# Kernel tuning notes

Hardware: AMD Instinct MI355X
Metric: run time of the kernel (lower is better)

The kernel has to match this reference:

```python
import jax, jax.numpy as jnp
import numpy as np

N_GRAPHS = 32
N_NODES = 2048          # nodes per graph == lstm1 input_size
N_TOTAL = N_GRAPHS * N_NODES
N_EDGES = 1048576
HEADS = 8
GAT_OUT = 12            # per-head GAT output dim (== num_features)
OUT_CH = 9
NEG_SLOPE = 0.2
BN_EPS = 1e-5


def setup_inputs() -> dict:
    key = jax.random.key(0)
    ks = jax.random.split(key, 20)
    inp = {}
    inp['x'] = jax.random.normal(ks[0], (N_TOTAL, GAT_OUT), jnp.float32)
    inp['edge_index'] = jax.random.randint(ks[1], (2, N_EDGES), 0, N_TOTAL, jnp.int64)
    inp['W_gat'] = jax.random.normal(ks[2], (GAT_OUT, HEADS * GAT_OUT), jnp.float32) * 0.3
    inp['a_src'] = jax.random.normal(ks[3], (HEADS, GAT_OUT), jnp.float32) * 0.3
    inp['a_dst'] = jax.random.normal(ks[4], (HEADS, GAT_OUT), jnp.float32) * 0.3
    inp['gat_bias'] = jax.random.normal(ks[5], (GAT_OUT,), jnp.float32) * 0.1
    inp['bn_gamma'] = jax.random.uniform(ks[6], (GAT_OUT,), jnp.float32, 0.5, 1.5)
    inp['bn_beta'] = jax.random.normal(ks[7], (GAT_OUT,), jnp.float32) * 0.1
    inp['bn_mean'] = jax.random.normal(ks[8], (GAT_OUT,), jnp.float32) * 0.1
    inp['bn_var'] = jax.random.uniform(ks[9], (GAT_OUT,), jnp.float32, 0.5, 1.5)
    inp['w_ih1'] = jax.random.normal(ks[10], (4 * 32, N_NODES), jnp.float32) / np.sqrt(N_NODES)
    inp['w_hh1'] = jax.random.normal(ks[11], (4 * 32, 32), jnp.float32) / np.sqrt(32)
    inp['b_ih1'] = jnp.zeros((4 * 32,), jnp.float32)
    inp['b_hh1'] = jnp.zeros((4 * 32,), jnp.float32)
    inp['w_ih2'] = jax.random.normal(ks[12], (4 * 128, 32), jnp.float32) / np.sqrt(32)
    inp['w_hh2'] = jax.random.normal(ks[13], (4 * 128, 128), jnp.float32) / np.sqrt(128)
    inp['b_ih2'] = jnp.zeros((4 * 128,), jnp.float32)
    inp['b_hh2'] = jnp.zeros((4 * 128,), jnp.float32)
    inp['lin_w'] = jax.random.normal(ks[14], (N_NODES, 128), jnp.float32) / np.sqrt(128)
    inp['lin_b'] = jax.random.normal(ks[15], (N_NODES,), jnp.float32) * 0.1
    return inp


def _gat(x, edge_index, W, a_src, a_dst, bias):
    # PyG GATConv, heads=HEADS, out=GAT_OUT, concat=False (mean over heads), eval mode.
    N = x.shape[0]
    xp = (x @ W).reshape(N, HEADS, GAT_OUT)               # [N,H,C]
    loops = jnp.arange(N, dtype=edge_index.dtype)
    src = jnp.concatenate([edge_index[0], loops])
    dst = jnp.concatenate([edge_index[1], loops])
    asrc = jnp.einsum('nhc,hc->nh', xp, a_src)            # [N,H]
    adst = jnp.einsum('nhc,hc->nh', xp, a_dst)
    e = jax.nn.leaky_relu(asrc[src] + adst[dst], NEG_SLOPE)  # [E,H]
    m = jax.ops.segment_max(e, dst, num_segments=N)
    e = jnp.exp(e - m[dst])
    denom = jax.ops.segment_sum(e, dst, num_segments=N)
    alpha = e / (denom[dst] + 1e-16)
    msg = xp[src] * alpha[:, :, None]                     # [E,H,C]
    out = jax.ops.segment_sum(msg, dst, num_segments=N)   # [N,H,C]
    return out.mean(axis=1) + bias                        # concat=False -> head mean


def _lstm(x_seq, w_ih, w_hh, b_ih, b_hh):
    # x_seq: [T,B,I]; PyTorch gate order i,f,g,o.
    Hh = w_hh.shape[1]
    B = x_seq.shape[1]
    bias = b_ih + b_hh

    def step(carry, xt):
        h, c = carry
        gates = xt @ w_ih.T + h @ w_hh.T + bias
        i, f, g, o = jnp.split(gates, 4, axis=-1)
        c = jax.nn.sigmoid(f) * c + jax.nn.sigmoid(i) * jnp.tanh(g)
        h = jax.nn.sigmoid(o) * jnp.tanh(c)
        return (h, c), h

    init = (jnp.zeros((B, Hh), x_seq.dtype), jnp.zeros((B, Hh), x_seq.dtype))
    _, hs = jax.lax.scan(step, init, x_seq)
    return hs


def reference(x, edge_index, W_gat, a_src, a_dst, gat_bias,
              bn_gamma, bn_beta, bn_mean, bn_var,
              w_ih1, w_hh1, b_ih1, b_hh1,
              w_ih2, w_hh2, b_ih2, b_hh2,
              lin_w, lin_b):
    h = _gat(x, edge_index, W_gat, a_src, a_dst, gat_bias)          # [N,12]
    h = (h - bn_mean) / jnp.sqrt(bn_var + BN_EPS) * bn_gamma + bn_beta
    # dropout inactive in eval mode
    h = jax.nn.log_softmax(h, axis=1)
    h = h.reshape(N_GRAPHS, N_NODES, GAT_OUT)
    h = jnp.moveaxis(h, 2, 0)                                       # [T=12,B,n]
    h = _lstm(h, w_ih1, w_hh1, b_ih1, b_hh1)                        # [12,B,32]
    h = _lstm(h, w_ih2, w_hh2, b_ih2, b_hh2)                        # [12,B,128]
    h = h @ lin_w.T + lin_b                                         # [12,B,n]
    h = h[-OUT_CH:]                                                 # [9,B,n]
    h = jnp.moveaxis(h, 0, 2)                                       # [B,n,9]
    return h.reshape(N_GRAPHS * N_NODES, OUT_CH)
```

## Files before the change

kernel.cpp:

```cpp
#include <hip/hip_runtime.h>
#include <math.h>

#define N_EDGES_C 1048576
#define N_TOTAL_C 65536

typedef _Float16 h2v __attribute__((ext_vector_type(2)));
typedef int i4v __attribute__((ext_vector_type(4)));

#if defined(__has_builtin)
#if __has_builtin(__builtin_amdgcn_fdot2)
#define HAS_FDOT2 1
#endif
#endif

__device__ __forceinline__ float fdot2(h2v a, h2v b, float c) {
#ifdef HAS_FDOT2
    return __builtin_amdgcn_fdot2(a, b, c, false);
#else
    return c + (float)a.x * (float)b.x + (float)a.y * (float)b.y;
#endif
}

__device__ __forceinline__ float sigf(float x){ return 1.0f/(1.0f+expf(-x)); }
__device__ __forceinline__ float lrelu(float x){ return (x>=0.f)? x : 0.2f*x; }


__global__ void prep_kernel(const float* __restrict__ x, const float* __restrict__ Wg,
                            const float* __restrict__ a_src, const float* __restrict__ a_dst,
                            _Float16* __restrict__ xpp)
{
    int tid = threadIdx.x;
    __shared__ float Ws[12*96];
    __shared__ float as_s[96], ad_s[96];
    for (int i = tid; i < 1152; i += 256) Ws[i] = Wg[i];
    if (tid < 96) { as_s[tid] = a_src[tid]; ad_s[tid] = a_dst[tid]; }
    __syncthreads();
    int gid = blockIdx.x * 256 + tid;
    int n = gid >> 3;
    int h = gid & 7;
    const float4* xv = (const float4*)(x + (size_t)n * 12);
    float4 v0 = xv[0], v1 = xv[1], v2 = xv[2];
    float xr[12] = {v0.x,v0.y,v0.z,v0.w, v1.x,v1.y,v1.z,v1.w, v2.x,v2.y,v2.z,v2.w};
    float xp_[12];
    #pragma unroll
    for (int c = 0; c < 12; c++) {
        float acc = 0.f;
        #pragma unroll
        for (int k = 0; k < 12; k++) acc += xr[k] * Ws[k*96 + h*12 + c];
        xp_[c] = acc;
    }
    float sa = 0.f, sd = 0.f;
    #pragma unroll
    for (int c = 0; c < 12; c++) { sa += xp_[c]*as_s[h*12+c]; sd += xp_[c]*ad_s[h*12+c]; }
    union { _Float16 hh[16]; float ff[8]; float4 f4[2]; } s;
    #pragma unroll
    for (int c = 0; c < 12; c++) s.hh[c] = (_Float16)xp_[c];
    s.ff[6] = sa;
    s.ff[7] = sd;
    float4* o = (float4*)(xpp + (size_t)gid * 16);
    o[0] = s.f4[0];
    o[1] = s.f4[1];
}

__global__ __launch_bounds__(256)
void edge_hist(const int* __restrict__ ei, unsigned* __restrict__ cnt,
               unsigned* __restrict__ rank8)
{
    __shared__ unsigned hist[16384];
    int tid = threadIdx.x;
    int slice = blockIdx.x;
    for (int i = tid; i < 16384; i += 256) hist[i] = 0;
    __syncthreads();
    const i4v* dst4 = (const i4v*)(ei + N_EDGES_C) + slice*2048;
    for (int i = tid; i < 2048; i += 256) {
        i4v d = __builtin_nontemporal_load(&dst4[i]);
        int dd[4] = {d.x, d.y, d.z, d.w};
        unsigned packed = 0;
        #pragma unroll
        for (int j = 0; j < 4; j++) {
            int dj = dd[j];
            unsigned sh = (unsigned)(dj & 3) << 3;
            unsigned old = atomicAdd(&hist[dj >> 2], 1u << sh);
            packed |= ((old >> sh) & 0xffu) << (j*8);
        }
        __builtin_nontemporal_store(packed, &rank8[slice*2048 + i]);
    }
    __syncthreads();
    unsigned* cg = cnt + (size_t)slice*16384;
    for (int i = tid; i < 16384; i += 256) cg[i] = hist[i];
}

__global__ void slice_prefix(unsigned* __restrict__ cnt, int* __restrict__ deg)
{
    int w = blockIdx.x*256 + threadIdx.x;
    unsigned run = 0;
    unsigned* base = cnt + w;
    for (int s = 0; s < 128; s++) {
        unsigned v = base[(size_t)s*16384];
        base[(size_t)s*16384] = run;
        run += v;
    }
    ((int4*)deg)[w] = make_int4((int)(run & 255u), (int)((run >> 8) & 255u),
                                (int)((run >> 16) & 255u), (int)(run >> 24));
}

__global__ void scan_build(const int* __restrict__ deg, int* __restrict__ rowptr)
{
    __shared__ int sums[1024];
    int tid = threadIdx.x;
    int4 v[16];
    const int4* deg4 = (const int4*)deg;
    #pragma unroll
    for (int j = 0; j < 16; j++) v[j] = deg4[tid*16 + j];
    int s = 0;
    #pragma unroll
    for (int j = 0; j < 16; j++) s += v[j].x + v[j].y + v[j].z + v[j].w;
    sums[tid] = s;
    __syncthreads();
    for (int off = 1; off < 1024; off <<= 1) {
        int t = 0;
        if (tid >= off) t = sums[tid - off];
        __syncthreads();
        if (tid >= off) sums[tid] += t;
        __syncthreads();
    }
    int run = sums[tid] - s;
    int4* rp4 = (int4*)rowptr;
    #pragma unroll
    for (int j = 0; j < 16; j++) {
        int4 r;
        r.x = run; run += v[j].x;
        r.y = run; run += v[j].y;
        r.z = run; run += v[j].z;
        r.w = run; run += v[j].w;
        rp4[tid*16 + j] = r;
    }
    if (tid == 1023) rowptr[65536] = run;
}

__global__ void edge_scatter(const int* __restrict__ ei, const unsigned* __restrict__ rank8,
                             const unsigned* __restrict__ cnt, const int* __restrict__ rowptr,
                             int* __restrict__ csr)
{
    int g8 = blockIdx.x & 7;
    int slice = (blockIdx.x >> 3) & 127;
    int half = blockIdx.x >> 10;
    int base = slice*2048 + half*1024;
    const i4v* dst4 = (const i4v*)(ei + N_EDGES_C);
    const i4v* src4 = (const i4v*)ei;
    const unsigned* cslice = cnt + (size_t)slice*16384;
    for (int i = threadIdx.x; i < 1024; i += 256) {
        int idx = base + i;
        i4v d = __builtin_nontemporal_load(&dst4[idx]);
        i4v s = __builtin_nontemporal_load(&src4[idx]);
        unsigned r = __builtin_nontemporal_load(&rank8[idx]);
        int dd[4] = {d.x, d.y, d.z, d.w};
        int ss[4] = {s.x, s.y, s.z, s.w};
        #pragma unroll
        for (int j = 0; j < 4; j++) {
            int dj = dd[j];
            if ((dj >> 13) == g8) {
                unsigned word = cslice[dj >> 2];
                int so = (int)((word >> ((unsigned)(dj & 3) << 3)) & 0xffu);
                int rk = (int)((r >> (j*8)) & 0xffu);
                csr[rowptr[dj] + so + rk] = ss[j];
            }
        }
    }
}

__global__ void gat_aggregate(const _Float16* __restrict__ xpp,
                              const int* __restrict__ rowptr, const int* __restrict__ csr_src,
                              const float* __restrict__ gat_bias, const float* __restrict__ bn_gamma,
                              const float* __restrict__ bn_beta, const float* __restrict__ bn_mean,
                              const float* __restrict__ bn_var, float* __restrict__ seq)
{
    int gid = blockIdx.x * 256 + threadIdx.x;
    int n = gid >> 3;
    int h = gid & 7;

    float acc[12];
    float adst_n, d;
    {
        const float4* p = (const float4*)(xpp + (size_t)n*128 + h*16);
        float4 f0 = p[0], f1 = p[1];
        adst_n = f1.w;
        float w = __expf(lrelu(f1.z + adst_n));
        d = w;
        h2v c0 = __builtin_bit_cast(h2v, f0.x), c1 = __builtin_bit_cast(h2v, f0.y);
        h2v c2 = __builtin_bit_cast(h2v, f0.z), c3 = __builtin_bit_cast(h2v, f0.w);
        h2v c4 = __builtin_bit_cast(h2v, f1.x), c5 = __builtin_bit_cast(h2v, f1.y);
        acc[0]=w*(float)c0.x; acc[1]=w*(float)c0.y; acc[2]=w*(float)c1.x; acc[3]=w*(float)c1.y;
        acc[4]=w*(float)c2.x; acc[5]=w*(float)c2.y; acc[6]=w*(float)c3.x; acc[7]=w*(float)c3.y;
        acc[8]=w*(float)c4.x; acc[9]=w*(float)c4.y; acc[10]=w*(float)c5.x; acc[11]=w*(float)c5.y;
    }

    auto accum = [&](float4 f0, float4 f1) {
        float w = __expf(lrelu(f1.z + adst_n));
        d += w;
        h2v c0 = __builtin_bit_cast(h2v, f0.x), c1 = __builtin_bit_cast(h2v, f0.y);
        h2v c2 = __builtin_bit_cast(h2v, f0.z), c3 = __builtin_bit_cast(h2v, f0.w);
        h2v c4 = __builtin_bit_cast(h2v, f1.x), c5 = __builtin_bit_cast(h2v, f1.y);
        acc[0]+=w*(float)c0.x; acc[1]+=w*(float)c0.y; acc[2]+=w*(float)c1.x; acc[3]+=w*(float)c1.y;
        acc[4]+=w*(float)c2.x; acc[5]+=w*(float)c2.y; acc[6]+=w*(float)c3.x; acc[7]+=w*(float)c3.y;
        acc[8]+=w*(float)c4.x; acc[9]+=w*(float)c4.y; acc[10]+=w*(float)c5.x; acc[11]+=w*(float)c5.y;
    };

    int beg = rowptr[n], end = rowptr[n+1];
    const _Float16* xh = xpp + (size_t)h * 16;
    int i = beg;
    for (; i + 4 <= end; i += 4) {
        int s0 = csr_src[i+0];
        int s1 = csr_src[i+1];
        int s2 = csr_src[i+2];
        int s3 = csr_src[i+3];
        const float4* p0 = (const float4*)(xh + (size_t)s0*128);
        const float4* p1 = (const float4*)(xh + (size_t)s1*128);
        const float4* p2 = (const float4*)(xh + (size_t)s2*128);
        const float4* p3 = (const float4*)(xh + (size_t)s3*128);
        float4 a0 = p0[0], b0 = p0[1];
        float4 a1 = p1[0], b1 = p1[1];
        float4 a2 = p2[0], b2 = p2[1];
        float4 a3 = p3[0], b3 = p3[1];
        accum(a0, b0);
        accum(a1, b1);
        accum(a2, b2);
        accum(a3, b3);
    }
    for (; i < end; i++) {
        int src = csr_src[i];
        const float4* p = (const float4*)(xh + (size_t)src*128);
        float4 f0 = p[0], f1 = p[1];
        accum(f0, f1);
    }

    float inv = 1.0f / (d + 1e-16f);
    float res[12];
    #pragma unroll
    for (int c = 0; c < 12; c++) {
        float v = acc[c] * inv;
        v += __shfl_xor(v, 1);
        v += __shfl_xor(v, 2);
        v += __shfl_xor(v, 4);
        res[c] = v * 0.125f;
    }
    if (h == 0) {
        float vals[12];
        float mx = -1e30f;
        #pragma unroll
        for (int c = 0; c < 12; c++) {
            float v = res[c] + gat_bias[c];
            v = (v - bn_mean[c]) * rsqrtf(bn_var[c] + 1e-5f) * bn_gamma[c] + bn_beta[c];
            vals[c] = v;
            mx = fmaxf(mx, v);
        }
        float sum = 0.f;
        #pragma unroll
        for (int c = 0; c < 12; c++) sum += __expf(vals[c] - mx);
        float lse = __logf(sum) + mx;
        #pragma unroll
        for (int c = 0; c < 12; c++) seq[(size_t)c * N_TOTAL_C + n] = vals[c] - lse;
    }
}

__global__ void gemm_x1(const float* __restrict__ A, const float* __restrict__ B,
                        float* __restrict__ C)
{
    __shared__ float As[32][33], Bs[32][33];
    const int K = 2048, N = 128;
    int tid = threadIdx.x;
    int tx = tid & 31, ty = tid >> 5;
    int bm = blockIdx.x * 32, bn = blockIdx.y * 32;
    int kbase = blockIdx.z * 128;
    float acc[4] = {0.f,0.f,0.f,0.f};
    for (int kk = 0; kk < 128; kk += 32) {
        int k0 = kbase + kk;
        #pragma unroll
        for (int i = 0; i < 4; i++) {
            int r = ty + i*8;
            As[r][tx] = A[(size_t)(bm + r) * K + k0 + tx];
            Bs[r][tx] = B[(size_t)(bn + r) * K + k0 + tx];
        }
        __syncthreads();
        #pragma unroll
        for (int k = 0; k < 32; k++) {
            float bv = Bs[tx][k];
            #pragma unroll
            for (int i = 0; i < 4; i++) acc[i] += As[ty + i*8][k] * bv;
        }
        __syncthreads();
    }
    #pragma unroll
    for (int i = 0; i < 4; i++)
        atomicAdd(&C[(size_t)(bm + ty + i*8) * N + bn + tx], acc[i]);
}

__global__ __launch_bounds__(512)
void lstm_fused(const float* __restrict__ X1, const float* __restrict__ w_hh1,
                const float* __restrict__ b_ih1, const float* __restrict__ b_hh1,
                const float* __restrict__ w_ih2, const float* __restrict__ w_hh2,
                const float* __restrict__ b_ih2, const float* __restrict__ b_hh2,
                float* __restrict__ H2)
{
    __shared__ float whh1[128*33];
    __shared__ float b1s[128];
    __shared__ float h1[32], c1[32];
    __shared__ __align__(16) _Float16 h1s[32];
    __shared__ __align__(16) _Float16 h2s[128];
    __shared__ float c2[128];
    __shared__ float g1s[128], g2s[512];
    int tid = threadIdx.x;
    int b = blockIdx.x;

    h2v whh[64];
    {
        const float2* wh = (const float2*)(w_hh2 + (size_t)tid * 128);
        #pragma unroll
        for (int k = 0; k < 64; k++) {
            float2 v = wh[k];
            h2v t; t.x = (_Float16)v.x; t.y = (_Float16)v.y;
            whh[k] = t;
        }
    }
    h2v wih[16];
    {
        const float2* wi = (const float2*)(w_ih2 + (size_t)tid * 32);
        #pragma unroll
        for (int k = 0; k < 16; k++) {
            float2 v = wi[k];
            h2v t; t.x = (_Float16)v.x; t.y = (_Float16)v.y;
            wih[k] = t;
        }
    }
    float b2 = b_ih2[tid] + b_hh2[tid];

    for (int i = tid; i < 128*32; i += 512) whh1[(i >> 5)*33 + (i & 31)] = w_hh1[i];
    if (tid < 128) b1s[tid] = b_ih1[tid] + b_hh1[tid];
    if (tid < 32)  { h1[tid] = 0.f; c1[tid] = 0.f; h1s[tid] = (_Float16)0.f; }
    if (tid < 128) { c2[tid] = 0.f; h2s[tid] = (_Float16)0.f; }
    __syncthreads();

    for (int t = 0; t < 12; t++) {
        float p0 = b2, p1 = 0.f, p2 = 0.f, p3 = 0.f;
        #pragma unroll
        for (int j = 0; j < 16; j++) {
            float4 f = ((const float4*)h2s)[j];
            p0 = fdot2(__builtin_bit_cast(h2v, f.x), whh[j*4+0], p0);
            p1 = fdot2(__builtin_bit_cast(h2v, f.y), whh[j*4+1], p1);
            p2 = fdot2(__builtin_bit_cast(h2v, f.z), whh[j*4+2], p2);
            p3 = fdot2(__builtin_bit_cast(h2v, f.w), whh[j*4+3], p3);
        }
        float acc2 = (p0 + p1) + (p2 + p3);

        if (tid < 128) {
            const float* wr = &whh1[tid * 33];
            float acc = X1[((size_t)t*32 + b)*128 + tid] + b1s[tid];
            #pragma unroll
            for (int k = 0; k < 32; k++) acc += h1[k] * wr[k];
            g1s[tid] = acc;
        }
        __syncthreads();
        if (tid < 32) {
            float ig = sigf(g1s[tid]), fg = sigf(g1s[32+tid]);
            float gg = tanhf(g1s[64+tid]), og = sigf(g1s[96+tid]);
            float cn = fg * c1[tid] + ig * gg;
            c1[tid] = cn;
            float hn = og * tanhf(cn);
            h1[tid] = hn;
            h1s[tid] = (_Float16)hn;
        }
        __syncthreads();
        {
            float q0 = 0.f, q1 = 0.f, q2 = 0.f, q3 = 0.f;
            #pragma unroll
            for (int j = 0; j < 4; j++) {
                float4 f = ((const float4*)h1s)[j];
                q0 = fdot2(__builtin_bit_cast(h2v, f.x), wih[j*4+0], q0);
                q1 = fdot2(__builtin_bit_cast(h2v, f.y), wih[j*4+1], q1);
                q2 = fdot2(__builtin_bit_cast(h2v, f.z), wih[j*4+2], q2);
                q3 = fdot2(__builtin_bit_cast(h2v, f.w), wih[j*4+3], q3);
            }
            g2s[tid] = acc2 + (q0 + q1) + (q2 + q3);
        }
        __syncthreads();
        if (tid < 128) {
            float ig = sigf(g2s[tid]), fg = sigf(g2s[128+tid]);
            float gg = tanhf(g2s[256+tid]), og = sigf(g2s[384+tid]);
            float cn = fg * c2[tid] + ig * gg;
            c2[tid] = cn;
            float hn = og * tanhf(cn);
            h2s[tid] = (_Float16)hn;
            if (t >= 3) H2[((size_t)t*32 + b)*128 + tid] = hn;
        }
        __syncthreads();
    }
}

__global__ void gemm_out(const float* __restrict__ A, const float* __restrict__ B,
                         const float* __restrict__ bias, float* __restrict__ out)
{
    __shared__ float As[32][33], Bs[32][33];
    const int K = 128;
    int tid = threadIdx.x;
    int tx = tid & 31, ty = tid >> 5;
    int bm = blockIdx.x * 32, bn = blockIdx.y * 32;
    float acc[4] = {0.f,0.f,0.f,0.f};
    for (int k0 = 0; k0 < K; k0 += 32) {
        #pragma unroll
        for (int i = 0; i < 4; i++) {
            int r = ty + i*8;
            As[r][tx] = A[(size_t)(bm + r) * K + k0 + tx];
            Bs[r][tx] = B[(size_t)(bn + r) * K + k0 + tx];
        }
        __syncthreads();
        #pragma unroll
        for (int kk = 0; kk < 32; kk++) {
            float bv = Bs[tx][kk];
            #pragma unroll
            for (int i = 0; i < 4; i++) acc[i] += As[ty + i*8][kk] * bv;
        }
        __syncthreads();
    }
    int j = blockIdx.x;
    int nn = bn + tx;
    float bv = bias[nn];
    #pragma unroll
    for (int i = 0; i < 4; i++) {
        int bb = ty + i*8;
        out[((size_t)bb * 2048 + nn) * 9 + j] = acc[i] + bv;
    }
}

extern "C" void kernel_launch(void* const* d_in, const int* in_sizes, int n_in,
                              void* d_out, int out_size, void* d_ws, size_t ws_size,
                              hipStream_t stream)
{
    const float* x        = (const float*)d_in[0];
    const int*   ei       = (const int*)  d_in[1];
    const float* W_gat    = (const float*)d_in[2];
    const float* a_src    = (const float*)d_in[3];
    const float* a_dst    = (const float*)d_in[4];
    const float* gat_bias = (const float*)d_in[5];
    const float* bn_gamma = (const float*)d_in[6];
    const float* bn_beta  = (const float*)d_in[7];
    const float* bn_mean  = (const float*)d_in[8];
    const float* bn_var   = (const float*)d_in[9];
    const float* w_ih1    = (const float*)d_in[10];
    const float* w_hh1    = (const float*)d_in[11];
    const float* b_ih1    = (const float*)d_in[12];
    const float* b_hh1    = (const float*)d_in[13];
    const float* w_ih2    = (const float*)d_in[14];
    const float* w_hh2    = (const float*)d_in[15];
    const float* b_ih2    = (const float*)d_in[16];
    const float* b_hh2    = (const float*)d_in[17];
    const float* lin_w    = (const float*)d_in[18];
    const float* lin_b    = (const float*)d_in[19];
    float* out = (float*)d_out;

    float* ws = (float*)d_ws;
    _Float16* xpp = (_Float16*)ws;
    float* seq  = ws + 4194304;
    float* X1   = seq + 786432;
    float* H2   = X1  + 49152;
    int* rowptr = (int*)(H2 + 49152);
    int* deg    = rowptr + 65544;
    unsigned* cnt = (unsigned*)(deg + 65536);
    unsigned* rank8 = cnt + 2097152;
    int* csr    = (int*)(rank8 + 262144);

    hipMemsetAsync(X1, 0, 49152 * sizeof(float), stream);
    prep_kernel <<<2048, 256, 0, stream>>>(x, W_gat, a_src, a_dst, xpp);
    edge_hist   <<<128, 256, 0, stream>>>(ei, cnt, rank8);
    slice_prefix<<<64, 256, 0, stream>>>(cnt, deg);
    scan_build  <<<1, 1024, 0, stream>>>(deg, rowptr);
    edge_scatter<<<2048, 256, 0, stream>>>(ei, rank8, cnt, rowptr, csr);
    gat_aggregate<<<2048, 256, 0, stream>>>(xpp, rowptr, csr,
                                            gat_bias, bn_gamma, bn_beta, bn_mean, bn_var, seq);
    gemm_x1<<<dim3(12, 4, 16), 256, 0, stream>>>(seq, w_ih1, X1);
    lstm_fused<<<32, 512, 0, stream>>>(X1, w_hh1, b_ih1, b_hh1, w_ih2, w_hh2, b_ih2, b_hh2, H2);
    gemm_out<<<dim3(9, 64), 256, 0, stream>>>(H2 + 96*128, lin_w, lin_b, out);
}
```

Measured before the change: 272.5 us.

## Stage edge scatter in LDS, prefetch LSTM inputs, use fast sigmoid/tanh

edge_scatter no longer has each of 8 group blocks re-read the same edges. Each block now reads its quarter-slice once, computes destination positions into shared memory tagged with a group id, then writes csr in 8 group-ordered passes. This cuts redundant global edge reads at the cost of LDS staging and a barrier. The LSTM kernel prefetches the next step's X1 value into a register and replaces expf/tanhf with __expf plus a hardware reciprocal, which lowers accuracy slightly. slice_prefix is relaunched with 128x128 threads instead of 64x256.

```diff
diff --git a/kernel.cpp b/kernel.cpp
--- a/kernel.cpp
+++ b/kernel.cpp
@@ -10,6 +10,9 @@
 #if defined(__has_builtin)
 #if __has_builtin(__builtin_amdgcn_fdot2)
 #define HAS_FDOT2 1
+#endif
+#if __has_builtin(__builtin_amdgcn_rcpf)
+#define HAS_RCPF 1
 #endif
 #endif
 
@@ -21,7 +24,15 @@
 #endif
 }
 
-__device__ __forceinline__ float sigf(float x){ return 1.0f/(1.0f+expf(-x)); }
+__device__ __forceinline__ float fast_rcp(float x) {
+#ifdef HAS_RCPF
+    return __builtin_amdgcn_rcpf(x);
+#else
+    return 1.0f / x;
+#endif
+}
+__device__ __forceinline__ float sigf(float x){ return fast_rcp(1.0f + __expf(-x)); }
+__device__ __forceinline__ float tanh_fast(float x){ return fmaf(2.0f, fast_rcp(1.0f + __expf(-2.0f*x)), -1.0f); }
 __device__ __forceinline__ float lrelu(float x){ return (x>=0.f)? x : 0.2f*x; }
 
 
@@ -92,7 +103,7 @@
 
 __global__ void slice_prefix(unsigned* __restrict__ cnt, int* __restrict__ deg)
 {
-    int w = blockIdx.x*256 + threadIdx.x;
+    int w = blockIdx.x*128 + threadIdx.x;
     unsigned run = 0;
     unsigned* base = cnt + w;
     for (int s = 0; s < 128; s++) {
@@ -138,18 +149,20 @@
     if (tid == 1023) rowptr[65536] = run;
 }
 
-__global__ void edge_scatter(const int* __restrict__ ei, const unsigned* __restrict__ rank8,
-                             const unsigned* __restrict__ cnt, const int* __restrict__ rowptr,
-                             int* __restrict__ csr)
-{
-    int g8 = blockIdx.x & 7;
-    int slice = (blockIdx.x >> 3) & 127;
-    int half = blockIdx.x >> 10;
-    int base = slice*2048 + half*1024;
+__global__ __launch_bounds__(256)
+void edge_scatter(const int* __restrict__ ei, const unsigned* __restrict__ rank8,
+                  const unsigned* __restrict__ cnt, const int* __restrict__ rowptr,
+                  int* __restrict__ csr)
+{
+    __shared__ unsigned pos_s[2048];
+    __shared__ int src_s[2048];
+    int slice = blockIdx.x >> 2;
+    int quar  = blockIdx.x & 3;
+    int base = slice*2048 + quar*512;
     const i4v* dst4 = (const i4v*)(ei + N_EDGES_C);
     const i4v* src4 = (const i4v*)ei;
     const unsigned* cslice = cnt + (size_t)slice*16384;
-    for (int i = threadIdx.x; i < 1024; i += 256) {
+    for (int i = threadIdx.x; i < 512; i += 256) {
         int idx = base + i;
         i4v d = __builtin_nontemporal_load(&dst4[idx]);
         i4v s = __builtin_nontemporal_load(&src4[idx]);
@@ -159,12 +172,20 @@
         #pragma unroll
         for (int j = 0; j < 4; j++) {
             int dj = dd[j];
-            if ((dj >> 13) == g8) {
-                unsigned word = cslice[dj >> 2];
-                int so = (int)((word >> ((unsigned)(dj & 3) << 3)) & 0xffu);
-                int rk = (int)((r >> (j*8)) & 0xffu);
-                csr[rowptr[dj] + so + rk] = ss[j];
-            }
+            unsigned word = cslice[dj >> 2];
+            int so = (int)((word >> ((unsigned)(dj & 3) << 3)) & 0xffu);
+            int rk = (int)((r >> (j*8)) & 0xffu);
+            unsigned pos = (unsigned)(rowptr[dj] + so + rk);
+            pos_s[i*4 + j] = pos | ((unsigned)(dj >> 13) << 24);
+            src_s[i*4 + j] = ss[j];
+        }
+    }
+    __syncthreads();
+    #pragma unroll 1
+    for (unsigned g = 0; g < 8; g++) {
+        for (int e = threadIdx.x; e < 2048; e += 256) {
+            unsigned pw = pos_s[e];
+            if ((pw >> 24) == g) csr[pw & 0xFFFFFFu] = src_s[e];
         }
     }
 }
@@ -338,9 +359,15 @@
     if (tid < 128) b1s[tid] = b_ih1[tid] + b_hh1[tid];
     if (tid < 32)  { h1[tid] = 0.f; c1[tid] = 0.f; h1s[tid] = (_Float16)0.f; }
     if (tid < 128) { c2[tid] = 0.f; h2s[tid] = (_Float16)0.f; }
+
+    float xv = 0.f;
+    if (tid < 128) xv = X1[((size_t)0*32 + b)*128 + tid];
     __syncthreads();
 
     for (int t = 0; t < 12; t++) {
+        float xv_next = 0.f;
+        if (t < 11 && tid < 128) xv_next = X1[((size_t)(t+1)*32 + b)*128 + tid];
+
         float p0 = b2, p1 = 0.f, p2 = 0.f, p3 = 0.f;
         #pragma unroll
         for (int j = 0; j < 16; j++) {
@@ -354,7 +381,7 @@
 
         if (tid < 128) {
             const float* wr = &whh1[tid * 33];
-            float acc = X1[((size_t)t*32 + b)*128 + tid] + b1s[tid];
+            float acc = xv + b1s[tid];
             #pragma unroll
             for (int k = 0; k < 32; k++) acc += h1[k] * wr[k];
             g1s[tid] = acc;
@@ -362,10 +389,10 @@
         __syncthreads();
         if (tid < 32) {
             float ig = sigf(g1s[tid]), fg = sigf(g1s[32+tid]);
-            float gg = tanhf(g1s[64+tid]), og = sigf(g1s[96+tid]);
+            float gg = tanh_fast(g1s[64+tid]), og = sigf(g1s[96+tid]);
             float cn = fg * c1[tid] + ig * gg;
             c1[tid] = cn;
-            float hn = og * tanhf(cn);
+            float hn = og * tanh_fast(cn);
             h1[tid] = hn;
             h1s[tid] = (_Float16)hn;
         }
@@ -385,14 +412,15 @@
         __syncthreads();
         if (tid < 128) {
             float ig = sigf(g2s[tid]), fg = sigf(g2s[128+tid]);
-            float gg = tanhf(g2s[256+tid]), og = sigf(g2s[384+tid]);
+            float gg = tanh_fast(g2s[256+tid]), og = sigf(g2s[384+tid]);
             float cn = fg * c2[tid] + ig * gg;
             c2[tid] = cn;
-            float hn = og * tanhf(cn);
+            float hn = og * tanh_fast(cn);
             h2s[tid] = (_Float16)hn;
             if (t >= 3) H2[((size_t)t*32 + b)*128 + tid] = hn;
         }
         __syncthreads();
+        xv = xv_next;
     }
 }
 
@@ -471,9 +499,9 @@
     hipMemsetAsync(X1, 0, 49152 * sizeof(float), stream);
     prep_kernel <<<2048, 256, 0, stream>>>(x, W_gat, a_src, a_dst, xpp);
     edge_hist   <<<128, 256, 0, stream>>>(ei, cnt, rank8);
-    slice_prefix<<<64, 256, 0, stream>>>(cnt, deg);
+    slice_prefix<<<128, 128, 0, stream>>>(cnt, deg);
     scan_build  <<<1, 1024, 0, stream>>>(deg, rowptr);
-    edge_scatter<<<2048, 256, 0, stream>>>(ei, rank8, cnt, rowptr, csr);
+    edge_scatter<<<512, 256, 0, stream>>>(ei, rank8, cnt, rowptr, csr);
     gat_aggregate<<<2048, 256, 0, stream>>>(xpp, rowptr, csr,
                                             gat_bias, bn_gamma, bn_beta, bn_mean, bn_var, seq);
     gemm_x1<<<dim3(12, 4, 16), 256, 0, stream>>>(seq, w_ih1, X1);
```

Measured after the change: 254.5 us. 1.07x faster.
